# Kernel optimization log

Hardware: AMD Instinct MI355X
Metric: run time of the kernel (lower is better)

The kernel has to match this reference:

```python
import jax, jax.numpy as jnp
import numpy as np

NUM_CLASSES = 3
POS_T, NEG_T = 0.5, 0.3
RATIO = 3
W_OBJ, W_CLS, W_LOC = 1.0, 1.0, 2.0


def _pairwise_iou(a, b):
    # a: [N,4] anchors, b: [G,4] gt boxes, xyxy
    ix1 = jnp.maximum(a[:, None, 0], b[None, :, 0])
    iy1 = jnp.maximum(a[:, None, 1], b[None, :, 1])
    ix2 = jnp.minimum(a[:, None, 2], b[None, :, 2])
    iy2 = jnp.minimum(a[:, None, 3], b[None, :, 3])
    inter = jnp.clip(ix2 - ix1, 0) * jnp.clip(iy2 - iy1, 0)
    area_a = (a[:, 2] - a[:, 0]) * (a[:, 3] - a[:, 1])
    area_b = (b[:, 2] - b[:, 0]) * (b[:, 3] - b[:, 1])
    union = area_a[:, None] + area_b[None, :] - inter
    return inter / jnp.maximum(union, 1e-9)


def _masked_mean(x, m):
    c = m.sum()
    return jnp.where(c > 0, (x * m).sum() / jnp.maximum(c, 1.0), 0.0)


def _per_image(pred, anc, ax, ay, aw, ah, boxes_gt, labels_gt):
    # pred: [N, 5+nc]; anc: [N,4]; boxes_gt: [G,4]; labels_gt: [G] in 1..nc
    iou = _pairwise_iou(anc, boxes_gt)              # [N, G]
    best = jnp.argmax(iou, axis=1)
    best_iou = jnp.max(iou, axis=1)
    pos = best_iou >= POS_T
    neg = best_iou < NEG_T
    mb = boxes_gt[best]                             # matched boxes [N,4]
    ml = labels_gt[best]                            # matched labels [N]
    obj_logit = pred[:, 4]
    cls_logit = pred[:, 5:]
    obj_t = pos.astype(pred.dtype)
    # BCEWithLogits (numerically stable)
    obj_loss = jnp.maximum(obj_logit, 0) - obj_logit * obj_t + jnp.log1p(jnp.exp(-jnp.abs(obj_logit)))
    # hard negative mining: top-(3*num_pos) detached obj losses among negatives
    num_pos = pos.sum()
    k = jnp.minimum(RATIO * num_pos, neg.sum())
    cand = jnp.where(neg, jax.lax.stop_gradient(obj_loss), -1.0)
    order = jnp.argsort(-cand)
    ranks = jnp.zeros_like(order).at[order].set(jnp.arange(order.shape[0], dtype=order.dtype))
    sel_neg = neg & (ranks < k)
    loss_obj = _masked_mean(obj_loss, (pos | sel_neg).astype(pred.dtype))
    # classification over positives, labels shifted to 0-based
    logp = jax.nn.log_softmax(cls_logit, axis=-1)
    tgt = jnp.clip(ml - 1, 0)
    ce = -jnp.take_along_axis(logp, tgt[:, None], axis=1)[:, 0]
    loss_cls = _masked_mean(ce, pos.astype(pred.dtype))
    # localization over positives: SmoothL1 on encoded offsets
    gx = (mb[:, 0] + mb[:, 2]) * 0.5
    gy = (mb[:, 1] + mb[:, 3]) * 0.5
    gw = jnp.maximum(mb[:, 2] - mb[:, 0], 1e-6)
    gh = jnp.maximum(mb[:, 3] - mb[:, 1], 1e-6)
    loc_tgt = jnp.stack([(gx - ax) / aw, (gy - ay) / ah,
                         jnp.log(gw / aw), jnp.log(gh / ah)], axis=1)
    d = pred[:, :4] - loc_tgt
    ad = jnp.abs(d)
    sl1 = jnp.where(ad < 1.0, 0.5 * d * d, ad - 0.5)  # [N,4]
    pm = pos.astype(pred.dtype)
    cnt = 4.0 * pm.sum()
    loss_loc = jnp.where(cnt > 0, (sl1 * pm[:, None]).sum() / jnp.maximum(cnt, 1.0), 0.0)
    return loss_obj, loss_cls, loss_loc


def _detection_loss(preds, ancs, gt_boxes, gt_labels):
    B = preds[0].shape[0]
    obj_s = 0.0
    cls_s = 0.0
    loc_s = 0.0
    for pred, anc in zip(preds, ancs):
        Bp, C, H, W = pred.shape
        p = jnp.transpose(pred, (0, 2, 3, 1)).reshape(Bp, -1, 5 + NUM_CLASSES)
        ax = (anc[:, 0] + anc[:, 2]) * 0.5
        ay = (anc[:, 1] + anc[:, 3]) * 0.5
        aw = jnp.maximum(anc[:, 2] - anc[:, 0], 1e-6)
        ah = jnp.maximum(anc[:, 3] - anc[:, 1], 1e-6)
        lo, lc, ll = jax.vmap(
            lambda pb, bb, lb: _per_image(pb, anc, ax, ay, aw, ah, bb, lb)
        )(p, gt_boxes, gt_labels)
        obj_s = obj_s + lo.sum()
        cls_s = cls_s + lc.sum()
        loc_s = loc_s + ll.sum()
    obj_m = obj_s / B
    cls_m = cls_s / B
    loc_m = loc_s / B
    total = W_OBJ * obj_m + W_CLS * cls_m + W_LOC * loc_m
    return total, obj_m, cls_m, loc_m


def setup_inputs() -> dict:
    key = jax.random.key(0)
    k = jax.random.split(key, 8)
    B, G, A = 32, 50, 3
    img = 512.0
    scales = [(128, 128), (64, 64), (32, 32)]
    C = A * (5 + NUM_CLASSES)  # 24

    def make_anchors(H, W):
        stride = img / H
        ys, xs = np.meshgrid(np.arange(H), np.arange(W), indexing="ij")
        cx = (xs + 0.5) * stride
        cy = (ys + 0.5) * stride
        per = []
        for s in (1.0, 1.5, 2.0):
            half = s * stride
            per.append(np.stack([cx - half, cy - half, cx + half, cy + half], axis=-1).reshape(-1, 4))
        b = np.stack(per, axis=1).reshape(-1, 4)  # [H*W*A, 4], A innermost
        return jnp.asarray(b, dtype=jnp.float32)

    preds = [jax.random.normal(k[i], (B, C, H, W), dtype=jnp.float32) for i, (H, W) in enumerate(scales)]
    ancs = [make_anchors(H, W) for (H, W) in scales]
    cx = jax.random.uniform(k[3], (B, G)) * 384.0 + 64.0
    cy = jax.random.uniform(k[4], (B, G)) * 384.0 + 64.0
    w = jax.random.uniform(k[5], (B, G)) * 112.0 + 16.0
    h = jax.random.uniform(k[6], (B, G)) * 112.0 + 16.0
    gt_boxes = jnp.stack([cx - w / 2, cy - h / 2, cx + w / 2, cy + h / 2], axis=-1).astype(jnp.float32)
    gt_labels = jax.random.randint(k[7], (B, G), 1, NUM_CLASSES + 1)
    return {"p0": preds[0], "p1": preds[1], "p2": preds[2],
            "a0": ancs[0], "a1": ancs[1], "a2": ancs[2],
            "gt_boxes": gt_boxes, "gt_labels": gt_labels}


def reference(p0, p1, p2, a0, a1, a2, gt_boxes, gt_labels):
    return _detection_loss([p0, p1, p2], [a0, a1, a2], gt_boxes, gt_labels)
```

## Files before the change

kernel.cpp:

```cpp
#include <hip/hip_runtime.h>

#define WS_ACC_POS   0
#define WS_ACC_NEG   96
#define WS_ACC_OBJ   192
#define WS_ACC_CLS   288
#define WS_ACC_LOC   384
#define WS_H1C       512
#define WS_H1S       (512 + 96*2048)
#define WS_TOTAL_U32 (512 + 2*96*2048)

__device__ __forceinline__ float sl1f(float d){
  float ad = fabsf(d); return ad < 1.f ? 0.5f*d*d : ad - 0.5f;
}
__device__ __forceinline__ unsigned int rec_cnt(unsigned int v){
  return (v >= 0xA0000000u) ? (v - 0xAAAAAAAAu) : v;
}

__global__ __launch_bounds__(256) void k_main(
    const float* __restrict__ p0, const float* __restrict__ p1, const float* __restrict__ p2,
    const float* __restrict__ gtb, const int* __restrict__ gtl,
    unsigned int* __restrict__ ws)
{
  const int id = blockIdx.x;
  int s, bIm, chunk, H, lw; const float* p;
  if (id < 2048){ s=0; H=128; lw=7; chunk=id>>5;            bIm=id&31;          p=p0; }
  else if (id < 2560){ s=1; H=64; lw=6; chunk=(id-2048)>>5; bIm=(id-2048)&31;   p=p1; }
  else {              s=2; H=32; lw=5; chunk=(id-2560)>>5;  bIm=(id-2560)&31;   p=p2; }
  const int W = H, HW = H*W;
  const float stride = 512.0f/(float)H;
  const int g = s*32 + bIm;
  const int tid = threadIdx.x;

  __shared__ float4 sBox[52];
  __shared__ float  sArea[52], sGx[52], sGy[52], sGw[52], sGh[52];
  __shared__ int    sLbl[52];
  __shared__ int    sNk;
  __shared__ unsigned int sHc[2048];
  __shared__ float        sHs[2048];
  __shared__ float  sRF[3][4];
  __shared__ unsigned int sRU[2][4];

  if (tid < 64){
    const int ymin = (chunk*256)>>lw;
    const int rowc = 256>>lw;
    const float by1 = ((float)ymin+0.5f)*stride - 2.0f*stride;
    const float by2 = ((float)(ymin+rowc-1)+0.5f)*stride + 2.0f*stride;
    bool keep=false; float4 gb=make_float4(0,0,0,0); int lbl=0;
    if (tid < 50){
      gb  = *(const float4*)(gtb + ((size_t)bIm*50 + tid)*4);
      lbl = gtl[bIm*50 + tid];
      keep = (fminf(by2, gb.w) - fmaxf(by1, gb.y)) > 0.f;
    }
    unsigned long long m = __ballot(keep);
    if (keep){
      int idx = __popcll(m & ((1ull<<tid)-1ull));
      sBox[idx]=gb;
      sArea[idx]=(gb.z-gb.x)*(gb.w-gb.y);
      sGx[idx]=(gb.x+gb.z)*0.5f;  sGy[idx]=(gb.y+gb.w)*0.5f;
      sGw[idx]=fmaxf(gb.z-gb.x,1e-6f); sGh[idx]=fmaxf(gb.w-gb.y,1e-6f);
      sLbl[idx]=lbl;
    }
    if (tid==0) sNk = __popcll(m);
  }
  for (int h=tid; h<2048; h+=256){ sHc[h]=0u; sHs[h]=0.f; }
  __syncthreads();

  const int nk = sNk;
  const int hw  = chunk*256 + tid;
  const int hwW = chunk*256 + (tid & ~63);
  const int y = hw>>lw, x = hw&(W-1);
  const float cx = ((float)x+0.5f)*stride, cy = ((float)y+0.5f)*stride;

  const int wxlo = (W >= 64) ? (hwW & (W-1)) : 0;
  const int wxhi = (W >= 64) ? (wxlo + 63)   : (W-1);
  const int wylo = hwW>>lw, wyhi = (hwW+63)>>lw;
  const float m2 = 2.0f*stride;
  const float wx1 = ((float)wxlo+0.5f)*stride - m2;
  const float wx2 = ((float)wxhi+0.5f)*stride + m2;
  const float wy1 = ((float)wylo+0.5f)*stride - m2;
  const float wy2 = ((float)wyhi+0.5f)*stride + m2;

  float half[3]; half[0]=stride; half[1]=1.5f*stride; half[2]=2.0f*stride;
  float areaA[3], bi[3], bu[3]; int bj[3];
  #pragma unroll
  for (int a=0;a<3;a++){
    const float aw = 2.0f*half[a];
    areaA[a]=aw*aw; bi[a]=0.f; bu[a]=1e-9f; bj[a]=0;
  }
  for (int j=0;j<nk;j++){
    const float4 gb = sBox[j];
    if (gb.x >= wx2 || gb.z <= wx1 || gb.y >= wy2 || gb.w <= wy1) continue;
    const float ar = sArea[j];
    #pragma unroll
    for (int a=0;a<3;a++){
      const float iy1 = fmaxf(cy-half[a], gb.y), iy2 = fminf(cy+half[a], gb.w);
      const float ih  = fmaxf(iy2-iy1, 0.f);
      const float ix1 = fmaxf(cx-half[a], gb.x), ix2 = fminf(cx+half[a], gb.z);
      const float iw  = fmaxf(ix2-ix1, 0.f);
      const float inter = iw*ih;
      const float un = areaA[a] + ar - inter;
      if (inter*bu[a] > bi[a]*un){ bi[a]=inter; bu[a]=un; bj[a]=j; }
    }
  }

  int accPos=0, accNeg=0;
  float accObj=0.f, accCls=0.f, accLoc=0.f;
  const float* pb = p + (size_t)bIm*24*HW + hw;
  #pragma unroll
  for (int a=0;a<3;a++){
    const float bestIou = bi[a]/bu[a];
    const bool pos = bestIou >= 0.5f;
    const bool neg = bestIou < 0.3f;
    const float xo = pb[(size_t)(a*8+4)*HW];
    float objl = fmaxf(xo,0.f) - (pos ? xo : 0.f)
               + __logf(1.f + __expf(-fabsf(xo)));
    objl = fmaxf(objl, 0.f);
    if (neg){
      accNeg++;
      const unsigned int bin = min(__float_as_uint(objl)>>20, 2047u);
      atomicAdd(&sHc[bin], 1u);
      atomicAdd(&sHs[bin], objl);
    }
    if (pos){
      accPos++; accObj += objl;
      const int jb = bj[a];
      const float aw = 2.0f*half[a];
      const float c0=pb[(size_t)(a*8+5)*HW], c1=pb[(size_t)(a*8+6)*HW], c2=pb[(size_t)(a*8+7)*HW];
      const float mm = fmaxf(fmaxf(c0,c1),c2);
      const float lse = mm + __logf(__expf(c0-mm)+__expf(c1-mm)+__expf(c2-mm));
      const int t = max(sLbl[jb]-1, 0);
      const float ct = (t==0)?c0 : (t==1)?c1 : c2;
      accCls += lse - ct;
      const float tx = (sGx[jb]-cx)/aw;
      const float ty = (sGy[jb]-cy)/aw;
      const float tw = __logf(sGw[jb]/aw);
      const float th = __logf(sGh[jb]/aw);
      accLoc += sl1f(pb[(size_t)(a*8+0)*HW]-tx) + sl1f(pb[(size_t)(a*8+1)*HW]-ty)
              + sl1f(pb[(size_t)(a*8+2)*HW]-tw) + sl1f(pb[(size_t)(a*8+3)*HW]-th);
    }
  }

  #pragma unroll
  for (int o=32;o;o>>=1){
    accPos += __shfl_down(accPos,o,64);
    accNeg += __shfl_down(accNeg,o,64);
    accObj += __shfl_down(accObj,o,64);
    accCls += __shfl_down(accCls,o,64);
    accLoc += __shfl_down(accLoc,o,64);
  }
  if ((tid & 63)==0){
    const int w = tid>>6;
    sRU[0][w]=(unsigned)accPos; sRU[1][w]=(unsigned)accNeg;
    sRF[0][w]=accObj; sRF[1][w]=accCls; sRF[2][w]=accLoc;
  }
  __syncthreads();
  if (tid==0){
    float* wf = (float*)ws;
    unsigned pc=0, nc=0; float ob=0,cl=0,lc=0;
    #pragma unroll
    for (int w=0;w<4;w++){ pc+=sRU[0][w]; nc+=sRU[1][w]; ob+=sRF[0][w]; cl+=sRF[1][w]; lc+=sRF[2][w]; }
    if (pc) atomicAdd(&ws[WS_ACC_POS+g], pc);
    if (nc) atomicAdd(&ws[WS_ACC_NEG+g], nc);
    if (ob!=0.f) atomicAdd(&wf[WS_ACC_OBJ+g], ob);
    if (cl!=0.f) atomicAdd(&wf[WS_ACC_CLS+g], cl);
    if (lc!=0.f) atomicAdd(&wf[WS_ACC_LOC+g], lc);
  }
  float* wf = (float*)ws;
  for (int h=tid; h<2048; h+=256){
    unsigned int v = sHc[h];
    if (v){
      atomicAdd(&ws[WS_H1C + g*2048 + h], v);
      atomicAdd(&wf[WS_H1S + g*2048 + h], sHs[h]);
    }
  }
}

__device__ __forceinline__ void wave_suffix_find(
    const unsigned int* __restrict__ binsLDS, const unsigned int* __restrict__ scC,
    unsigned int target, int* sTie, int* sR, int lane)
{
  const unsigned int c4 = scC[4*lane]+scC[4*lane+1]+scC[4*lane+2]+scC[4*lane+3];
  unsigned int incl = c4;
  #pragma unroll
  for (int off=1; off<64; off<<=1){
    unsigned int yv = __shfl_down(incl, off, 64);
    if (lane+off < 64) incl += yv;
  }
  const unsigned int excl = incl - c4;
  if (excl < target && incl >= target){
    unsigned int cum = excl; int fs = 4*lane;
    for (int ss=3; ss>=0; ss--){
      unsigned int c = scC[4*lane+ss];
      if (cum + c >= target){ fs = 4*lane+ss; break; }
      cum += c;
    }
    for (int bin=fs*8+7; bin>=fs*8; bin--){
      unsigned int c = binsLDS[bin];
      if (cum + c >= target){ *sTie = bin; *sR = (int)(target - cum); break; }
      cum += c;
    }
  }
}

__global__ __launch_bounds__(256) void k_select(unsigned int* __restrict__ ws,
                                                float* __restrict__ out){
  const int g = blockIdx.x, tid = threadIdx.x;
  float* wf = (float*)ws;
  __shared__ unsigned int hc[2048];
  __shared__ float        hs[2048];
  __shared__ unsigned int scC[256];
  __shared__ int sTie1, sR1;
  __shared__ float sRed[4];

  const int pos  = (int)rec_cnt(ws[WS_ACC_POS+g]);
  const int negc = (int)rec_cnt(ws[WS_ACC_NEG+g]);
  const int k = min(3*pos, negc);
  float selSum = 0.f;

  if (k > 0){
    #pragma unroll
    for (int i=0;i<8;i++){
      hc[tid+256*i] = rec_cnt(ws[WS_H1C + g*2048 + tid + 256*i]);
      hs[tid+256*i] = wf[WS_H1S + g*2048 + tid + 256*i];
    }
    __syncthreads();
    unsigned int sum=0;
    #pragma unroll
    for (int i=0;i<8;i++) sum += hc[tid*8+i];
    scC[tid]=sum;
    __syncthreads();
    if (tid < 64) wave_suffix_find(hc, scC, (unsigned)k, &sTie1, &sR1, tid);
    __syncthreads();
    const int tie1 = sTie1;
    float above = 0.f;
    #pragma unroll
    for (int i=0;i<8;i++){
      const int bin = tid*8+i;
      if (bin > tie1) above += hs[bin];
    }
    #pragma unroll
    for (int o=32;o;o>>=1) above += __shfl_down(above,o,64);
    if ((tid&63)==0) sRed[tid>>6] = above;
    __syncthreads();
    if (tid==0){
      const float ab = sRed[0]+sRed[1]+sRed[2]+sRed[3];
      selSum = ab + (float)sR1 * (hs[tie1]/(float)hc[tie1]);
    }
  }
  if (tid==0){
    const int cObj = pos + k;
    const float lo = (cObj>0) ? (wf[WS_ACC_OBJ+g]+selSum)/(float)cObj : 0.f;
    const float lc = (pos>0)  ? wf[WS_ACC_CLS+g]/(float)pos           : 0.f;
    const float ll = (pos>0)  ? wf[WS_ACC_LOC+g]/(float)(4*pos)       : 0.f;
    const float invB = 1.f/32.f;
    atomicAdd(out+0, (lo + lc + 2.f*ll)*invB);
    atomicAdd(out+1, lo*invB);
    atomicAdd(out+2, lc*invB);
    atomicAdd(out+3, ll*invB);
  }
}

extern "C" void kernel_launch(void* const* d_in, const int* in_sizes, int n_in,
                              void* d_out, int out_size, void* d_ws, size_t ws_size,
                              hipStream_t stream){
  if (ws_size < (size_t)WS_TOTAL_U32*4) return;
  const float* p0  = (const float*)d_in[0];
  const float* p1  = (const float*)d_in[1];
  const float* p2  = (const float*)d_in[2];
  const float* gtb = (const float*)d_in[6];
  const int*   gtl = (const int*)d_in[7];
  unsigned int* ws = (unsigned int*)d_ws;
  float* out = (float*)d_out;

  hipLaunchKernelGGL(k_main,   dim3(2688), dim3(256), 0, stream, p0,p1,p2,gtb,gtl,ws);
  hipLaunchKernelGGL(k_select, dim3(96),   dim3(256), 0, stream, ws, out);
}
```

Baseline: 132.0 us.

## Fuse main and select kernels via last-block completion counter, two rows per thread

Merges the per-anchor loss kernel and the hard-negative selection kernel into one launch. The last block for each group, detected with an atomic done counter, performs the histogram top-k selection. Each thread now handles two rows of anchors, which halves the block count and the per-block histogram flushes and reuses the x-direction IoU work across both rows. The cost is a serialized tail on the last block of each group, plus reliance on the workspace counters being in the expected initial state.

```diff
diff --git a/kernel.cpp b/kernel.cpp
--- a/kernel.cpp
+++ b/kernel.cpp
@@ -5,9 +5,10 @@
 #define WS_ACC_OBJ   192
 #define WS_ACC_CLS   288
 #define WS_ACC_LOC   384
-#define WS_H1C       512
-#define WS_H1S       (512 + 96*2048)
-#define WS_TOTAL_U32 (512 + 2*96*2048)
+#define WS_DONE      480
+#define WS_H1C       576
+#define WS_H1S       (576 + 96*2048)
+#define WS_TOTAL_U32 (576 + 2*96*2048)
 
 __device__ __forceinline__ float sl1f(float d){
   float ad = fabsf(d); return ad < 1.f ? 0.5f*d*d : ad - 0.5f;
@@ -15,21 +16,53 @@
 __device__ __forceinline__ unsigned int rec_cnt(unsigned int v){
   return (v >= 0xA0000000u) ? (v - 0xAAAAAAAAu) : v;
 }
-
-__global__ __launch_bounds__(256) void k_main(
+__device__ __forceinline__ unsigned int aload_u32(const unsigned int* p){
+  return __hip_atomic_load(p, __ATOMIC_RELAXED, __HIP_MEMORY_SCOPE_AGENT);
+}
+
+__device__ __forceinline__ void wave_suffix_find(
+    const unsigned int* __restrict__ binsLDS, const unsigned int* __restrict__ scC,
+    unsigned int target, int* sTie, int* sR, int lane)
+{
+  const unsigned int c4 = scC[4*lane]+scC[4*lane+1]+scC[4*lane+2]+scC[4*lane+3];
+  unsigned int incl = c4;
+  #pragma unroll
+  for (int off=1; off<64; off<<=1){
+    unsigned int yv = __shfl_down(incl, off, 64);
+    if (lane+off < 64) incl += yv;
+  }
+  const unsigned int excl = incl - c4;
+  if (excl < target && incl >= target){
+    unsigned int cum = excl; int fs = 4*lane;
+    for (int ss=3; ss>=0; ss--){
+      unsigned int c = scC[4*lane+ss];
+      if (cum + c >= target){ fs = 4*lane+ss; break; }
+      cum += c;
+    }
+    for (int bin=fs*8+7; bin>=fs*8; bin--){
+      unsigned int c = binsLDS[bin];
+      if (cum + c >= target){ *sTie = bin; *sR = (int)(target - cum); break; }
+      cum += c;
+    }
+  }
+}
+
+__global__ __launch_bounds__(256) void k_fused(
     const float* __restrict__ p0, const float* __restrict__ p1, const float* __restrict__ p2,
     const float* __restrict__ gtb, const int* __restrict__ gtl,
-    unsigned int* __restrict__ ws)
+    unsigned int* __restrict__ ws, float* __restrict__ out)
 {
   const int id = blockIdx.x;
-  int s, bIm, chunk, H, lw; const float* p;
-  if (id < 2048){ s=0; H=128; lw=7; chunk=id>>5;            bIm=id&31;          p=p0; }
-  else if (id < 2560){ s=1; H=64; lw=6; chunk=(id-2048)>>5; bIm=(id-2048)&31;   p=p1; }
-  else {              s=2; H=32; lw=5; chunk=(id-2560)>>5;  bIm=(id-2560)&31;   p=p2; }
+  int s, bIm, chunk, H, lw, nblk; const float* p;
+  if (id < 1024){ s=0; H=128; lw=7; chunk=id>>5;            bIm=id&31;          p=p0; nblk=32; }
+  else if (id < 1280){ s=1; H=64; lw=6; chunk=(id-1024)>>5; bIm=(id-1024)&31;   p=p1; nblk=8;  }
+  else {              s=2; H=32; lw=5; chunk=(id-1280)>>5;  bIm=(id-1280)&31;   p=p2; nblk=2;  }
   const int W = H, HW = H*W;
   const float stride = 512.0f/(float)H;
   const int g = s*32 + bIm;
   const int tid = threadIdx.x;
+  const int R  = 512>>lw;
+  const int r0 = chunk*R;
 
   __shared__ float4 sBox[52];
   __shared__ float  sArea[52], sGx[52], sGy[52], sGw[52], sGh[52];
@@ -39,12 +72,13 @@
   __shared__ float        sHs[2048];
   __shared__ float  sRF[3][4];
   __shared__ unsigned int sRU[2][4];
+  __shared__ unsigned int scC[256];
+  __shared__ int sLast, sTie1, sR1;
+  __shared__ float sRed[4];
 
   if (tid < 64){
-    const int ymin = (chunk*256)>>lw;
-    const int rowc = 256>>lw;
-    const float by1 = ((float)ymin+0.5f)*stride - 2.0f*stride;
-    const float by2 = ((float)(ymin+rowc-1)+0.5f)*stride + 2.0f*stride;
+    const float by1 = ((float)r0+0.5f)*stride - 2.0f*stride;
+    const float by2 = ((float)(r0+R-1)+0.5f)*stride + 2.0f*stride;
     bool keep=false; float4 gb=make_float4(0,0,0,0); int lbl=0;
     if (tid < 50){
       gb  = *(const float4*)(gtb + ((size_t)bIm*50 + tid)*4);
@@ -66,26 +100,31 @@
   __syncthreads();
 
   const int nk = sNk;
-  const int hw  = chunk*256 + tid;
-  const int hwW = chunk*256 + (tid & ~63);
-  const int y = hw>>lw, x = hw&(W-1);
-  const float cx = ((float)x+0.5f)*stride, cy = ((float)y+0.5f)*stride;
-
-  const int wxlo = (W >= 64) ? (hwW & (W-1)) : 0;
-  const int wxhi = (W >= 64) ? (wxlo + 63)   : (W-1);
-  const int wylo = hwW>>lw, wyhi = (hwW+63)>>lw;
+  const int x  = tid & (W-1);
+  const int y0 = r0 + ((tid>>lw)<<1);
+  const int hwA = y0*W + x;
+  const float cx  = ((float)x +0.5f)*stride;
+  const float cy0 = ((float)y0+0.5f)*stride;
+
+  const int tidW = tid & ~63;
+  const int xlo = (W >= 64) ? (tidW & (W-1)) : 0;
+  const int xhi = (W >= 64) ? (xlo + 63)     : (W-1);
+  const int ylo = r0 + ((tidW>>lw)<<1);
+  const int yhi = r0 + (((tidW+63)>>lw)<<1) + 1;
   const float m2 = 2.0f*stride;
-  const float wx1 = ((float)wxlo+0.5f)*stride - m2;
-  const float wx2 = ((float)wxhi+0.5f)*stride + m2;
-  const float wy1 = ((float)wylo+0.5f)*stride - m2;
-  const float wy2 = ((float)wyhi+0.5f)*stride + m2;
+  const float wx1 = ((float)xlo+0.5f)*stride - m2;
+  const float wx2 = ((float)xhi+0.5f)*stride + m2;
+  const float wy1 = ((float)ylo+0.5f)*stride - m2;
+  const float wy2 = ((float)yhi+0.5f)*stride + m2;
 
   float half[3]; half[0]=stride; half[1]=1.5f*stride; half[2]=2.0f*stride;
-  float areaA[3], bi[3], bu[3]; int bj[3];
+  float areaA[3], bi[2][3], bu[2][3]; int bj[2][3];
   #pragma unroll
   for (int a=0;a<3;a++){
     const float aw = 2.0f*half[a];
-    areaA[a]=aw*aw; bi[a]=0.f; bu[a]=1e-9f; bj[a]=0;
+    areaA[a]=aw*aw;
+    #pragma unroll
+    for (int rr=0;rr<2;rr++){ bi[rr][a]=0.f; bu[rr][a]=1e-9f; bj[rr][a]=0; }
   }
   for (int j=0;j<nk;j++){
     const float4 gb = sBox[j];
@@ -93,50 +132,59 @@
     const float ar = sArea[j];
     #pragma unroll
     for (int a=0;a<3;a++){
-      const float iy1 = fmaxf(cy-half[a], gb.y), iy2 = fminf(cy+half[a], gb.w);
-      const float ih  = fmaxf(iy2-iy1, 0.f);
       const float ix1 = fmaxf(cx-half[a], gb.x), ix2 = fminf(cx+half[a], gb.z);
       const float iw  = fmaxf(ix2-ix1, 0.f);
-      const float inter = iw*ih;
-      const float un = areaA[a] + ar - inter;
-      if (inter*bu[a] > bi[a]*un){ bi[a]=inter; bu[a]=un; bj[a]=j; }
+      #pragma unroll
+      for (int rr=0;rr<2;rr++){
+        const float cyr = cy0 + (float)rr*stride;
+        const float iy1 = fmaxf(cyr-half[a], gb.y), iy2 = fminf(cyr+half[a], gb.w);
+        const float ih  = fmaxf(iy2-iy1, 0.f);
+        const float inter = iw*ih;
+        const float un = areaA[a] + ar - inter;
+        if (inter*bu[rr][a] > bi[rr][a]*un){ bi[rr][a]=inter; bu[rr][a]=un; bj[rr][a]=j; }
+      }
     }
   }
 
   int accPos=0, accNeg=0;
   float accObj=0.f, accCls=0.f, accLoc=0.f;
-  const float* pb = p + (size_t)bIm*24*HW + hw;
-  #pragma unroll
-  for (int a=0;a<3;a++){
-    const float bestIou = bi[a]/bu[a];
-    const bool pos = bestIou >= 0.5f;
-    const bool neg = bestIou < 0.3f;
-    const float xo = pb[(size_t)(a*8+4)*HW];
-    float objl = fmaxf(xo,0.f) - (pos ? xo : 0.f)
-               + __logf(1.f + __expf(-fabsf(xo)));
-    objl = fmaxf(objl, 0.f);
-    if (neg){
-      accNeg++;
-      const unsigned int bin = min(__float_as_uint(objl)>>20, 2047u);
-      atomicAdd(&sHc[bin], 1u);
-      atomicAdd(&sHs[bin], objl);
-    }
-    if (pos){
-      accPos++; accObj += objl;
-      const int jb = bj[a];
-      const float aw = 2.0f*half[a];
-      const float c0=pb[(size_t)(a*8+5)*HW], c1=pb[(size_t)(a*8+6)*HW], c2=pb[(size_t)(a*8+7)*HW];
-      const float mm = fmaxf(fmaxf(c0,c1),c2);
-      const float lse = mm + __logf(__expf(c0-mm)+__expf(c1-mm)+__expf(c2-mm));
-      const int t = max(sLbl[jb]-1, 0);
-      const float ct = (t==0)?c0 : (t==1)?c1 : c2;
-      accCls += lse - ct;
-      const float tx = (sGx[jb]-cx)/aw;
-      const float ty = (sGy[jb]-cy)/aw;
-      const float tw = __logf(sGw[jb]/aw);
-      const float th = __logf(sGh[jb]/aw);
-      accLoc += sl1f(pb[(size_t)(a*8+0)*HW]-tx) + sl1f(pb[(size_t)(a*8+1)*HW]-ty)
-              + sl1f(pb[(size_t)(a*8+2)*HW]-tw) + sl1f(pb[(size_t)(a*8+3)*HW]-th);
+  const float* pb = p + (size_t)bIm*24*HW;
+  #pragma unroll
+  for (int rr=0;rr<2;rr++){
+    const int hw = hwA + rr*W;
+    const float cyr = cy0 + (float)rr*stride;
+    #pragma unroll
+    for (int a=0;a<3;a++){
+      const float bestIou = bi[rr][a]/bu[rr][a];
+      const bool pos = bestIou >= 0.5f;
+      const bool neg = bestIou < 0.3f;
+      const float xo = pb[(size_t)(a*8+4)*HW + hw];
+      float objl = fmaxf(xo,0.f) - (pos ? xo : 0.f)
+                 + __logf(1.f + __expf(-fabsf(xo)));
+      objl = fmaxf(objl, 0.f);
+      if (neg){
+        accNeg++;
+        const unsigned int bin = min(__float_as_uint(objl)>>20, 2047u);
+        atomicAdd(&sHc[bin], 1u);
+        atomicAdd(&sHs[bin], objl);
+      }
+      if (pos){
+        accPos++; accObj += objl;
+        const int jb = bj[rr][a];
+        const float aw = 2.0f*half[a];
+        const float c0=pb[(size_t)(a*8+5)*HW+hw], c1=pb[(size_t)(a*8+6)*HW+hw], c2=pb[(size_t)(a*8+7)*HW+hw];
+        const float mm = fmaxf(fmaxf(c0,c1),c2);
+        const float lse = mm + __logf(__expf(c0-mm)+__expf(c1-mm)+__expf(c2-mm));
+        const int t = max(sLbl[jb]-1, 0);
+        const float ct = (t==0)?c0 : (t==1)?c1 : c2;
+        accCls += lse - ct;
+        const float tx = (sGx[jb]-cx )/aw;
+        const float ty = (sGy[jb]-cyr)/aw;
+        const float tw = __logf(sGw[jb]/aw);
+        const float th = __logf(sGh[jb]/aw);
+        accLoc += sl1f(pb[(size_t)(a*8+0)*HW+hw]-tx) + sl1f(pb[(size_t)(a*8+1)*HW+hw]-ty)
+                + sl1f(pb[(size_t)(a*8+2)*HW+hw]-tw) + sl1f(pb[(size_t)(a*8+3)*HW+hw]-th);
+      }
     }
   }
 
@@ -154,8 +202,8 @@
     sRF[0][w]=accObj; sRF[1][w]=accCls; sRF[2][w]=accLoc;
   }
   __syncthreads();
+  float* wf = (float*)ws;
   if (tid==0){
-    float* wf = (float*)ws;
     unsigned pc=0, nc=0; float ob=0,cl=0,lc=0;
     #pragma unroll
     for (int w=0;w<4;w++){ pc+=sRU[0][w]; nc+=sRU[1][w]; ob+=sRF[0][w]; cl+=sRF[1][w]; lc+=sRF[2][w]; }
@@ -165,7 +213,6 @@
     if (cl!=0.f) atomicAdd(&wf[WS_ACC_CLS+g], cl);
     if (lc!=0.f) atomicAdd(&wf[WS_ACC_LOC+g], lc);
   }
-  float* wf = (float*)ws;
   for (int h=tid; h<2048; h+=256){
     unsigned int v = sHc[h];
     if (v){
@@ -173,70 +220,42 @@
       atomicAdd(&wf[WS_H1S + g*2048 + h], sHs[h]);
     }
   }
-}
-
-__device__ __forceinline__ void wave_suffix_find(
-    const unsigned int* __restrict__ binsLDS, const unsigned int* __restrict__ scC,
-    unsigned int target, int* sTie, int* sR, int lane)
-{
-  const unsigned int c4 = scC[4*lane]+scC[4*lane+1]+scC[4*lane+2]+scC[4*lane+3];
-  unsigned int incl = c4;
-  #pragma unroll
-  for (int off=1; off<64; off<<=1){
-    unsigned int yv = __shfl_down(incl, off, 64);
-    if (lane+off < 64) incl += yv;
-  }
-  const unsigned int excl = incl - c4;
-  if (excl < target && incl >= target){
-    unsigned int cum = excl; int fs = 4*lane;
-    for (int ss=3; ss>=0; ss--){
-      unsigned int c = scC[4*lane+ss];
-      if (cum + c >= target){ fs = 4*lane+ss; break; }
-      cum += c;
-    }
-    for (int bin=fs*8+7; bin>=fs*8; bin--){
-      unsigned int c = binsLDS[bin];
-      if (cum + c >= target){ *sTie = bin; *sR = (int)(target - cum); break; }
-      cum += c;
-    }
-  }
-}
-
-__global__ __launch_bounds__(256) void k_select(unsigned int* __restrict__ ws,
-                                                float* __restrict__ out){
-  const int g = blockIdx.x, tid = threadIdx.x;
-  float* wf = (float*)ws;
-  __shared__ unsigned int hc[2048];
-  __shared__ float        hs[2048];
-  __shared__ unsigned int scC[256];
-  __shared__ int sTie1, sR1;
-  __shared__ float sRed[4];
-
-  const int pos  = (int)rec_cnt(ws[WS_ACC_POS+g]);
-  const int negc = (int)rec_cnt(ws[WS_ACC_NEG+g]);
+  __syncthreads();
+
+  if (tid==0){
+    __threadfence();
+    unsigned old = atomicAdd(&ws[WS_DONE+g], 1u);
+    sLast = (rec_cnt(old) == (unsigned)(nblk-1)) ? 1 : 0;
+  }
+  __syncthreads();
+  if (!sLast) return;
+  __threadfence();
+
+  const int pos  = (int)rec_cnt(aload_u32(&ws[WS_ACC_POS+g]));
+  const int negc = (int)rec_cnt(aload_u32(&ws[WS_ACC_NEG+g]));
   const int k = min(3*pos, negc);
   float selSum = 0.f;
 
   if (k > 0){
     #pragma unroll
     for (int i=0;i<8;i++){
-      hc[tid+256*i] = rec_cnt(ws[WS_H1C + g*2048 + tid + 256*i]);
-      hs[tid+256*i] = wf[WS_H1S + g*2048 + tid + 256*i];
+      sHc[tid+256*i] = rec_cnt(aload_u32(&ws[WS_H1C + g*2048 + tid + 256*i]));
+      sHs[tid+256*i] = __uint_as_float(aload_u32(&ws[WS_H1S + g*2048 + tid + 256*i]));
     }
     __syncthreads();
     unsigned int sum=0;
     #pragma unroll
-    for (int i=0;i<8;i++) sum += hc[tid*8+i];
+    for (int i=0;i<8;i++) sum += sHc[tid*8+i];
     scC[tid]=sum;
     __syncthreads();
-    if (tid < 64) wave_suffix_find(hc, scC, (unsigned)k, &sTie1, &sR1, tid);
+    if (tid < 64) wave_suffix_find(sHc, scC, (unsigned)k, &sTie1, &sR1, tid);
     __syncthreads();
     const int tie1 = sTie1;
     float above = 0.f;
     #pragma unroll
     for (int i=0;i<8;i++){
       const int bin = tid*8+i;
-      if (bin > tie1) above += hs[bin];
+      if (bin > tie1) above += sHs[bin];
     }
     #pragma unroll
     for (int o=32;o;o>>=1) above += __shfl_down(above,o,64);
@@ -244,14 +263,17 @@
     __syncthreads();
     if (tid==0){
       const float ab = sRed[0]+sRed[1]+sRed[2]+sRed[3];
-      selSum = ab + (float)sR1 * (hs[tie1]/(float)hc[tie1]);
+      selSum = ab + (float)sR1 * (sHs[tie1]/(float)sHc[tie1]);
     }
   }
   if (tid==0){
+    const float sObj = __uint_as_float(aload_u32(&ws[WS_ACC_OBJ+g]));
+    const float sCls = __uint_as_float(aload_u32(&ws[WS_ACC_CLS+g]));
+    const float sLoc = __uint_as_float(aload_u32(&ws[WS_ACC_LOC+g]));
     const int cObj = pos + k;
-    const float lo = (cObj>0) ? (wf[WS_ACC_OBJ+g]+selSum)/(float)cObj : 0.f;
-    const float lc = (pos>0)  ? wf[WS_ACC_CLS+g]/(float)pos           : 0.f;
-    const float ll = (pos>0)  ? wf[WS_ACC_LOC+g]/(float)(4*pos)       : 0.f;
+    const float lo = (cObj>0) ? (sObj+selSum)/(float)cObj : 0.f;
+    const float lc = (pos>0)  ? sCls/(float)pos           : 0.f;
+    const float ll = (pos>0)  ? sLoc/(float)(4*pos)       : 0.f;
     const float invB = 1.f/32.f;
     atomicAdd(out+0, (lo + lc + 2.f*ll)*invB);
     atomicAdd(out+1, lo*invB);
@@ -272,6 +294,6 @@
   unsigned int* ws = (unsigned int*)d_ws;
   float* out = (float*)d_out;
 
-  hipLaunchKernelGGL(k_main,   dim3(2688), dim3(256), 0, stream, p0,p1,p2,gtb,gtl,ws);
-  hipLaunchKernelGGL(k_select, dim3(96),   dim3(256), 0, stream, ws, out);
-}
+  hipLaunchKernelGGL(k_fused, dim3(1344), dim3(256), 0, stream,
+                     p0,p1,p2,gtb,gtl,ws,out);
+}
```

Result: slower. 149.3 us (+13.1%).
